# Optimization experiments

Measured on AMD Instinct MI355X. Metric: run time of the kernel, lower is better.

Reference implementation:

```python
import jax, jax.numpy as jnp
import numpy as np

PAD_TOKEN = -2.0
EPS = 1e-6
NEG_INF = -1.0e9


def _layer_norm(x, gamma, beta):
    mu = jnp.mean(x, axis=-1, keepdims=True)
    var = jnp.mean(jnp.square(x - mu), axis=-1, keepdims=True)
    return (x - mu) * jax.lax.rsqrt(var + EPS) * gamma + beta


def setup_inputs() -> dict:
    key = jax.random.key(0)
    ks = jax.random.split(key, 10)
    B, N, M, D, H, E, O = 128, 32, 384, 256, 8, 32, 256
    S = N + M
    x_pmhc = jax.random.normal(ks[0], (B, S, D), jnp.float32)
    # masks hold raw token values; PAD_TOKEN marks padding positions
    p_len = jax.random.randint(ks[1], (B,), 8, N + 1)
    m_len = jax.random.randint(ks[2], (B,), M // 2, M + 1)
    p_mask = jnp.where(jnp.arange(N)[None, :] < p_len[:, None], 1.0, PAD_TOKEN).astype(jnp.float32)
    m_mask = jnp.where(jnp.arange(M)[None, :] < m_len[:, None], 1.0, PAD_TOKEN).astype(jnp.float32)
    # learned params (keras random_normal init stddev=0.05; random_uniform in [-0.05, 0.05])
    q_proj = 0.05 * jax.random.normal(ks[3], (H, D, E), jnp.float32)
    k_proj = 0.05 * jax.random.normal(ks[4], (H, D, E), jnp.float32)
    v_proj = 0.05 * jax.random.normal(ks[5], (H, D, E), jnp.float32)
    g_proj = jax.random.uniform(ks[6], (H, D, E), jnp.float32, -0.05, 0.05)
    out_w = 0.05 * jax.random.normal(ks[7], (H * E, O), jnp.float32)
    out_b = jnp.zeros((O,), jnp.float32)
    ln1_g = jnp.ones((D,), jnp.float32)
    ln1_b = jnp.zeros((D,), jnp.float32)
    ln2_g = jnp.ones((O,), jnp.float32)
    ln2_b = jnp.zeros((O,), jnp.float32)
    return dict(x_pmhc=x_pmhc, p_mask=p_mask, m_mask=m_mask,
                q_proj=q_proj, k_proj=k_proj, v_proj=v_proj, g_proj=g_proj,
                out_w=out_w, out_b=out_b,
                ln1_g=ln1_g, ln1_b=ln1_b, ln2_g=ln2_g, ln2_b=ln2_b)


def _mask_2d(p, m):
    # p: [B,N] in {0,1}, m: [B,M] in {0,1}
    B, N = p.shape
    M = m.shape[1]
    cross_pm = p[:, :, None] * m[:, None, :]          # [B,N,M]
    cross_mp = m[:, :, None] * p[:, None, :]          # [B,M,N]
    top = jnp.concatenate([jnp.zeros((B, N, N), p.dtype), cross_pm], axis=2)
    bot = jnp.concatenate([cross_mp, jnp.zeros((B, M, M), p.dtype)], axis=2)
    return jnp.concatenate([top, bot], axis=1)        # [B,S,S]


def reference(x_pmhc, p_mask, m_mask, q_proj, k_proj, v_proj, g_proj,
              out_w, out_b, ln1_g, ln1_b, ln2_g, ln2_b):
    H, _, E = q_proj.shape
    B, S, _ = x_pmhc.shape
    scale = 1.0 / jnp.sqrt(jnp.asarray(E, jnp.float32))
    x = _layer_norm(x_pmhc, ln1_g, ln1_b)
    p = jnp.where(p_mask == PAD_TOKEN, 0.0, 1.0)
    m = jnp.where(m_mask == PAD_TOKEN, 0.0, 1.0)
    q = jnp.einsum('bxd,hde->bhxe', x, q_proj)
    k = jnp.einsum('bxd,hde->bhxe', x, k_proj)
    v = jnp.einsum('bxd,hde->bhxe', x, v_proj)
    g = jnp.einsum('bxd,hde->bhxe', x, g_proj)
    att = jnp.einsum('bhxe,bhye->bhxy', q, k) * scale          # [B,H,S,S]
    mask2d = _mask_2d(p, m)                                     # [B,S,S]
    att = jax.nn.softmax(att + ((1.0 - mask2d) * NEG_INF)[:, None], axis=-1)
    att = att * mask2d[:, None]
    out = jnp.einsum('bhxy,bhye->bhxe', att, v)
    out = out * jax.nn.sigmoid(g)
    out = out.transpose(0, 2, 1, 3).reshape(B, S, H * E)
    out = out @ out_w + out_b
    return _layer_norm(out, ln2_g, ln2_b)
```

## Files before the change

### kernel.cpp

```cpp
#include <hip/hip_runtime.h>

typedef unsigned short u16;
typedef __bf16 bf16x8 __attribute__((ext_vector_type(8)));
typedef float f32x4 __attribute__((ext_vector_type(4)));

#define B_    128
#define S_    416
#define NPEP  32
#define MMHC  384
#define D_    256
#define H_    8
#define E_    32
#define O_    256
#define BS_   (B_ * S_)

#define PAD_TOK (-2.0f)
#define SCALE_E 0.17677669529663687f

typedef const __attribute__((address_space(1))) void cg_void;
typedef __attribute__((address_space(3))) void lds_void;

__device__ __forceinline__ float bf2f(u16 u) {
  union { unsigned int i; float f; } x; x.i = ((unsigned int)u) << 16; return x.f;
}
__device__ __forceinline__ u16 f2bf(float f) {
  union { float f; unsigned int i; } x; x.f = f;
  unsigned int i = x.i;
  return (u16)((i + 0x7FFFu + ((i >> 16) & 1u)) >> 16);
}
__device__ __forceinline__ unsigned pk2bf(float lo, float hi) {
  return (unsigned)f2bf(lo) | ((unsigned)f2bf(hi) << 16);
}

__global__ __launch_bounds__(256)
void prep(const float* __restrict__ q, const float* __restrict__ k,
          const float* __restrict__ v, const float* __restrict__ g,
          const float* __restrict__ ow, u16* __restrict__ WT, u16* __restrict__ WoT,
          const float* __restrict__ x, u16* __restrict__ xln,
          const float* __restrict__ gam, const float* __restrict__ bet) {
  const int bx = blockIdx.x, t = threadIdx.x;
  if (bx < 1024) {
    const int col = bx;
    const int p = col >> 8, h = (col >> 5) & 7, e = col & 31;
    const float* src = (p == 0) ? q : (p == 1) ? k : (p == 2) ? v : g;
    WT[col * 256 + t] = f2bf(src[(h * 256 + t) * 32 + e]);
    return;
  }
  if (bx < 1280) {
    const int n = bx - 1024;
    WoT[n * 256 + t] = f2bf(ow[t * 256 + n]);
    return;
  }
  const int w = t >> 6, lane = t & 63;
  const size_t row = (size_t)(bx - 1280) * 4 + w;
  const float4 u = *((const float4*)x + row * 64 + lane);
  const float x0 = u.x, x1 = u.y, x2 = u.z, x3 = u.w;
  float sum = (x0 + x1) + (x2 + x3);
  float ss  = (x0 * x0 + x1 * x1) + (x2 * x2 + x3 * x3);
  #pragma unroll
  for (int off = 32; off; off >>= 1) {
    sum += __shfl_xor(sum, off);
    ss  += __shfl_xor(ss, off);
  }
  const float mean = sum * 0.00390625f;
  float var = ss * 0.00390625f - mean * mean;
  var = fmaxf(var, 0.0f);
  const float rs = rsqrtf(var + 1e-6f);
  const float4 g4 = *((const float4*)gam + lane);
  const float4 b4 = *((const float4*)bet + lane);
  ushort4 r;
  r.x = f2bf((x0 - mean) * rs * g4.x + b4.x);
  r.y = f2bf((x1 - mean) * rs * g4.y + b4.y);
  r.z = f2bf((x2 - mean) * rs * g4.z + b4.z);
  r.w = f2bf((x3 - mean) * rs * g4.w + b4.w);
  *((ushort4*)xln + row * 64 + lane) = r;
}

__global__ __launch_bounds__(256, 2)
void gemm_qkvg(const u16* __restrict__ A, const u16* __restrict__ BT,
               u16* __restrict__ Qh, u16* __restrict__ Kh,
               u16* __restrict__ Vh, u16* __restrict__ Gh) {
  __shared__ __attribute__((aligned(16))) u16 As[2][128 * 64];
  __shared__ __attribute__((aligned(16))) u16 Bs[2][128 * 64];
  const int L = blockIdx.x;
  const int m0 = ((L & 7) + 8 * (L >> 6)) * 128;
  const int n0 = ((L >> 3) & 7) * 128;
  const int tid = threadIdx.x;
  const int lane = tid & 63;
  const int w = tid >> 6;
  const int wr = (w >> 1) * 64;
  const int wc = (w & 1) * 64;
  const int mi = lane & 15;
  const int quad = lane >> 4;
  const int rseg = lane >> 3;
  const int gcol = (lane & 7) ^ rseg;

#define STAGE_G1(buf, kc)                                                      \
  {                                                                            \
    _Pragma("unroll")                                                          \
    for (int j = 0; j < 4; ++j) {                                              \
      const int seg = w * 4 + j;                                               \
      const int r = seg * 8 + rseg;                                            \
      const u16* ga = &A[(size_t)(m0 + r) * 256 + (kc) + gcol * 8];            \
      __builtin_amdgcn_global_load_lds((cg_void*)ga,                           \
          (lds_void*)&As[buf][seg * 512], 16, 0, 0);                           \
      const u16* gb = &BT[(size_t)(n0 + r) * 256 + (kc) + gcol * 8];           \
      __builtin_amdgcn_global_load_lds((cg_void*)gb,                           \
          (lds_void*)&Bs[buf][seg * 512], 16, 0, 0);                           \
    }                                                                          \
  }

  f32x4 acc[4][4] = {};
  STAGE_G1(0, 0);
  __syncthreads();
  #pragma unroll
  for (int kt8 = 0; kt8 < 4; ++kt8) {
    const int cur = kt8 & 1;
    if (kt8 < 3) STAGE_G1(cur ^ 1, (kt8 + 1) * 64);
    #pragma unroll
    for (int kt = 0; kt < 2; ++kt) {
      bf16x8 a[4], bb[4];
      #pragma unroll
      for (int i = 0; i < 4; ++i) {
        const int m = wr + i * 16 + mi;
        const int pg = (kt * 4 + quad) ^ (mi & 7);
        a[i] = *(const bf16x8*)&As[cur][m * 64 + pg * 8];
      }
      #pragma unroll
      for (int i = 0; i < 4; ++i) {
        const int n = wc + i * 16 + mi;
        const int pg = (kt * 4 + quad) ^ (mi & 7);
        bb[i] = *(const bf16x8*)&Bs[cur][n * 64 + pg * 8];
      }
      #pragma unroll
      for (int i = 0; i < 4; ++i)
        #pragma unroll
        for (int jn = 0; jn < 4; ++jn)
          acc[i][jn] = __builtin_amdgcn_mfma_f32_16x16x32_bf16(a[i], bb[jn], acc[i][jn], 0, 0, 0);
    }
    if (kt8 < 3) __syncthreads();
  }
#undef STAGE_G1
  u16* dstj[4];
  #pragma unroll
  for (int jn = 0; jn < 4; ++jn) {
    const int colb = n0 + wc + jn * 16;
    const int p = colb >> 8;
    const int h = (colb >> 5) & 7;
    const int e = (colb & 16) + mi;
    u16* bp = (p == 0) ? Qh : (p == 1) ? Kh : (p == 2) ? Vh : Gh;
    dstj[jn] = bp + (size_t)h * BS_ * 32 + e;
  }
  #pragma unroll
  for (int i = 0; i < 4; ++i) {
    const int row = m0 + wr + i * 16 + quad * 4;
    #pragma unroll
    for (int r = 0; r < 4; ++r) {
      #pragma unroll
      for (int jn = 0; jn < 4; ++jn)
        dstj[jn][(size_t)(row + r) * 32] = f2bf(acc[i][jn][r]);
    }
  }
}

__global__ __launch_bounds__(256, 4)
void att_fused(const u16* __restrict__ Qh, const u16* __restrict__ Kh,
               const u16* __restrict__ Vh, const u16* __restrict__ Gh,
               const float* __restrict__ p_mask, const float* __restrict__ m_mask,
               u16* __restrict__ atto) {
  __shared__ __attribute__((aligned(16))) u16 VT[32][392];
  __shared__ __attribute__((aligned(16))) u16 VpT[32][40];
  __shared__ __attribute__((aligned(16))) float pf[32];
  __shared__ __attribute__((aligned(16))) float mfl[384];
  const int bh = blockIdx.x;
  const int b = bh >> 3, h = bh & 7;
  const int t = threadIdx.x;
  const int lane = t & 63, w = t >> 6;
  const int mi = lane & 15, quad = lane >> 4;
  const size_t hb = (size_t)h * BS_ + (size_t)b * S_;

  if (t < 32) pf[t] = (p_mask[b * NPEP + t] == PAD_TOK) ? 0.0f : 1.0f;
  mfl[t] = (m_mask[b * MMHC + t] == PAD_TOK) ? 0.0f : 1.0f;
  if (t < 128) mfl[256 + t] = (m_mask[b * MMHC + 256 + t] == PAD_TOK) ? 0.0f : 1.0f;
  {
    const int y = t >> 3, e0 = (t & 7) * 4;
    const ushort4 u = *(const ushort4*)&Vh[(hb + y) * 32 + e0];
    VpT[e0 + 0][y] = u.x; VpT[e0 + 1][y] = u.y;
    VpT[e0 + 2][y] = u.z; VpT[e0 + 3][y] = u.w;
  }
  #pragma unroll
  for (int i = 0; i < 12; ++i) {
    const int idx = i * 256 + t;
    const int y = idx >> 3, e0 = (idx & 7) * 4;
    const ushort4 u = *(const ushort4*)&Vh[(hb + 32 + y) * 32 + e0];
    VT[e0 + 0][y] = u.x; VT[e0 + 1][y] = u.y;
    VT[e0 + 2][y] = u.z; VT[e0 + 3][y] = u.w;
  }
  __syncthreads();

  const f32x4 fz = {0.0f, 0.0f, 0.0f, 0.0f};
  const int idxA = ((quad & 1) * 2) * 16 + mi;
  const int idxB = idxA + 16;
  const bool hi = quad >= 2;
  union U8 { unsigned u[4]; bf16x8 v; };

  if (w < 2) {
    const bf16x8 aq = *(const bf16x8*)&Qh[(hb + w * 16 + mi) * 32 + quad * 8];
    float lsum = 0.0f;
    f32x4 o0 = fz, o1 = fz;
    #pragma unroll
    for (int ks = 0; ks < 12; ++ks) {
      unsigned pA0, pA1, pB0, pB1;
      {
        const int kt = 2 * ks;
        const bf16x8 bk = *(const bf16x8*)&Kh[(hb + 32 + kt * 16 + mi) * 32 + quad * 8];
        const f32x4 s = __builtin_amdgcn_mfma_f32_16x16x32_bf16(bk, aq, fz, 0, 0, 0);
        const float4 m4 = *(const float4*)&mfl[kt * 16 + quad * 4];
        const float e0 = m4.x * __expf(s[0] * SCALE_E);
        const float e1 = m4.y * __expf(s[1] * SCALE_E);
        const float e2 = m4.z * __expf(s[2] * SCALE_E);
        const float e3 = m4.w * __expf(s[3] * SCALE_E);
        lsum += (e0 + e1) + (e2 + e3);
        pA0 = pk2bf(e0, e1); pA1 = pk2bf(e2, e3);
      }
      {
        const int kt = 2 * ks + 1;
        const bf16x8 bk = *(const bf16x8*)&Kh[(hb + 32 + kt * 16 + mi) * 32 + quad * 8];
        const f32x4 s = __builtin_amdgcn_mfma_f32_16x16x32_bf16(bk, aq, fz, 0, 0, 0);
        const float4 m4 = *(const float4*)&mfl[kt * 16 + quad * 4];
        const float e0 = m4.x * __expf(s[0] * SCALE_E);
        const float e1 = m4.y * __expf(s[1] * SCALE_E);
        const float e2 = m4.z * __expf(s[2] * SCALE_E);
        const float e3 = m4.w * __expf(s[3] * SCALE_E);
        lsum += (e0 + e1) + (e2 + e3);
        pB0 = pk2bf(e0, e1); pB1 = pk2bf(e2, e3);
      }
      const unsigned a00 = __shfl(pA0, idxA), a01 = __shfl(pA1, idxA);
      const unsigned b00 = __shfl(pB0, idxA), b01 = __shfl(pB1, idxA);
      const unsigned a10 = __shfl(pA0, idxB), a11 = __shfl(pA1, idxB);
      const unsigned b10 = __shfl(pB0, idxB), b11 = __shfl(pB1, idxB);
      U8 pf_;
      pf_.u[0] = hi ? b00 : a00;
      pf_.u[1] = hi ? b01 : a01;
      pf_.u[2] = hi ? b10 : a10;
      pf_.u[3] = hi ? b11 : a11;
      const bf16x8 v0 = *(const bf16x8*)&VT[mi][ks * 32 + quad * 8];
      const bf16x8 v1 = *(const bf16x8*)&VT[16 + mi][ks * 32 + quad * 8];
      o0 = __builtin_amdgcn_mfma_f32_16x16x32_bf16(v0, pf_.v, o0, 0, 0, 0);
      o1 = __builtin_amdgcn_mfma_f32_16x16x32_bf16(v1, pf_.v, o1, 0, 0, 0);
    }
    lsum += __shfl_xor(lsum, 16);
    lsum += __shfl_xor(lsum, 32);
    const int prow = w * 16 + mi;
    const float sc = (1.0f / lsum) * pf[prow];
    const ushort4 g0 = *(const ushort4*)&Gh[(hb + prow) * 32 + quad * 4];
    const ushort4 g1 = *(const ushort4*)&Gh[(hb + prow) * 32 + 16 + quad * 4];
    ushort4 r0, r1;
    r0.x = f2bf(o0[0] * sc / (1.0f + __expf(-bf2f(g0.x))));
    r0.y = f2bf(o0[1] * sc / (1.0f + __expf(-bf2f(g0.y))));
    r0.z = f2bf(o0[2] * sc / (1.0f + __expf(-bf2f(g0.z))));
    r0.w = f2bf(o0[3] * sc / (1.0f + __expf(-bf2f(g0.w))));
    r1.x = f2bf(o1[0] * sc / (1.0f + __expf(-bf2f(g1.x))));
    r1.y = f2bf(o1[1] * sc / (1.0f + __expf(-bf2f(g1.y))));
    r1.z = f2bf(o1[2] * sc / (1.0f + __expf(-bf2f(g1.z))));
    r1.w = f2bf(o1[3] * sc / (1.0f + __expf(-bf2f(g1.w))));
    *(ushort4*)&atto[(hb + prow) * 32 + quad * 4] = r0;
    *(ushort4*)&atto[(hb + prow) * 32 + 16 + quad * 4] = r1;
  } else {
    const int wid = w - 2;
    const bf16x8 bk0 = *(const bf16x8*)&Kh[(hb + mi) * 32 + quad * 8];
    const bf16x8 bk1 = *(const bf16x8*)&Kh[(hb + 16 + mi) * 32 + quad * 8];
    const bf16x8 bv0 = *(const bf16x8*)&VpT[mi][quad * 8];
    const bf16x8 bv1 = *(const bf16x8*)&VpT[16 + mi][quad * 8];
    const float4 pfa = *(const float4*)&pf[quad * 4];
    const float4 pfb = *(const float4*)&pf[16 + quad * 4];
    for (int i = 0; i < 12; ++i) {
      const int rloc = (i * 2 + wid) * 16;
      const size_t grow = hb + 32 + rloc + mi;
      const bf16x8 aq = *(const bf16x8*)&Qh[grow * 32 + quad * 8];
      const f32x4 s0 = __builtin_amdgcn_mfma_f32_16x16x32_bf16(bk0, aq, fz, 0, 0, 0);
      const f32x4 s1 = __builtin_amdgcn_mfma_f32_16x16x32_bf16(bk1, aq, fz, 0, 0, 0);
      const float e00 = pfa.x * __expf(s0[0] * SCALE_E);
      const float e01 = pfa.y * __expf(s0[1] * SCALE_E);
      const float e02 = pfa.z * __expf(s0[2] * SCALE_E);
      const float e03 = pfa.w * __expf(s0[3] * SCALE_E);
      const float e10 = pfb.x * __expf(s1[0] * SCALE_E);
      const float e11 = pfb.y * __expf(s1[1] * SCALE_E);
      const float e12 = pfb.z * __expf(s1[2] * SCALE_E);
      const float e13 = pfb.w * __expf(s1[3] * SCALE_E);
      float lsum = ((e00 + e01) + (e02 + e03)) + ((e10 + e11) + (e12 + e13));
      lsum += __shfl_xor(lsum, 16);
      lsum += __shfl_xor(lsum, 32);
      const unsigned pA0 = pk2bf(e00, e01), pA1 = pk2bf(e02, e03);
      const unsigned pB0 = pk2bf(e10, e11), pB1 = pk2bf(e12, e13);
      const unsigned a00 = __shfl(pA0, idxA), a01 = __shfl(pA1, idxA);
      const unsigned b00 = __shfl(pB0, idxA), b01 = __shfl(pB1, idxA);
      const unsigned a10 = __shfl(pA0, idxB), a11 = __shfl(pA1, idxB);
      const unsigned b10 = __shfl(pB0, idxB), b11 = __shfl(pB1, idxB);
      U8 pf_;
      pf_.u[0] = hi ? b00 : a00;
      pf_.u[1] = hi ? b01 : a01;
      pf_.u[2] = hi ? b10 : a10;
      pf_.u[3] = hi ? b11 : a11;
      const f32x4 o0 = __builtin_amdgcn_mfma_f32_16x16x32_bf16(bv0, pf_.v, fz, 0, 0, 0);
      const f32x4 o1 = __builtin_amdgcn_mfma_f32_16x16x32_bf16(bv1, pf_.v, fz, 0, 0, 0);
      const float sc = (1.0f / lsum) * mfl[rloc + mi];
      const ushort4 g0 = *(const ushort4*)&Gh[grow * 32 + quad * 4];
      const ushort4 g1 = *(const ushort4*)&Gh[grow * 32 + 16 + quad * 4];
      ushort4 r0, r1;
      r0.x = f2bf(o0[0] * sc / (1.0f + __expf(-bf2f(g0.x))));
      r0.y = f2bf(o0[1] * sc / (1.0f + __expf(-bf2f(g0.y))));
      r0.z = f2bf(o0[2] * sc / (1.0f + __expf(-bf2f(g0.z))));
      r0.w = f2bf(o0[3] * sc / (1.0f + __expf(-bf2f(g0.w))));
      r1.x = f2bf(o1[0] * sc / (1.0f + __expf(-bf2f(g1.x))));
      r1.y = f2bf(o1[1] * sc / (1.0f + __expf(-bf2f(g1.y))));
      r1.z = f2bf(o1[2] * sc / (1.0f + __expf(-bf2f(g1.z))));
      r1.w = f2bf(o1[3] * sc / (1.0f + __expf(-bf2f(g1.w))));
      *(ushort4*)&atto[grow * 32 + quad * 4] = r0;
      *(ushort4*)&atto[grow * 32 + 16 + quad * 4] = r1;
    }
  }
}

__global__ __launch_bounds__(512, 2)
void gemm2_ln(const u16* __restrict__ A, const u16* __restrict__ BT,
              float* __restrict__ out, const float* __restrict__ bias,
              const float* __restrict__ gam, const float* __restrict__ bet) {
  __shared__ __attribute__((aligned(16))) u16 As[128 * 64];
  __shared__ __attribute__((aligned(16))) u16 Bs[256 * 64];
  __shared__ float rsum[128][4];
  __shared__ float rssq[128][4];
  __shared__ float mean_s[128], rstd_s[128];
  const int m0 = blockIdx.x * 128;
  const int tid = threadIdx.x;
  const int lane = tid & 63;
  const int w = tid >> 6;
  const int wr = (w >> 2) * 64;
  const int wc = (w & 3) * 64;
  const int mi = lane & 15;
  const int quad = lane >> 4;
  const int rseg = lane >> 3;
  const int gcol = (lane & 7) ^ rseg;
  f32x4 acc[4][4] = {};
  for (int kc = 0; kc < 256; kc += 64) {
    __syncthreads();
    #pragma unroll
    for (int j = 0; j < 2; ++j) {
      const int seg = w * 2 + j;
      const int r = seg * 8 + rseg;
      const int c = kc + gcol * 8;
      const u16* ga = &A[((size_t)(c >> 5) * BS_ + (m0 + r)) * 32 + (c & 31)];
      __builtin_amdgcn_global_load_lds((cg_void*)ga, (lds_void*)&As[seg * 512], 16, 0, 0);
    }
    #pragma unroll
    for (int j = 0; j < 4; ++j) {
      const int seg = w * 4 + j;
      const int r = seg * 8 + rseg;
      const u16* gb = &BT[(size_t)r * 256 + kc + gcol * 8];
      __builtin_amdgcn_global_load_lds((cg_void*)gb, (lds_void*)&Bs[seg * 512], 16, 0, 0);
    }
    __syncthreads();
    #pragma unroll
    for (int kt = 0; kt < 2; ++kt) {
      bf16x8 a[4], bb[4];
      #pragma unroll
      for (int i = 0; i < 4; ++i) {
        const int m = wr + i * 16 + mi;
        const int pg = (kt * 4 + quad) ^ (mi & 7);
        a[i] = *(const bf16x8*)&As[m * 64 + pg * 8];
      }
      #pragma unroll
      for (int i = 0; i < 4; ++i) {
        const int n = wc + i * 16 + mi;
        const int pg = (kt * 4 + quad) ^ (mi & 7);
        bb[i] = *(const bf16x8*)&Bs[n * 64 + pg * 8];
      }
      #pragma unroll
      for (int i = 0; i < 4; ++i)
        #pragma unroll
        for (int jn = 0; jn < 4; ++jn)
          acc[i][jn] = __builtin_amdgcn_mfma_f32_16x16x32_bf16(a[i], bb[jn], acc[i][jn], 0, 0, 0);
    }
  }
  float bia[4];
  #pragma unroll
  for (int jn = 0; jn < 4; ++jn) bia[jn] = bias[wc + jn * 16 + mi];
  #pragma unroll
  for (int i = 0; i < 4; ++i) {
    #pragma unroll
    for (int r = 0; r < 4; ++r) {
      float s = 0.0f, qq = 0.0f;
      #pragma unroll
      for (int jn = 0; jn < 4; ++jn) {
        const float v = acc[i][jn][r] + bia[jn];
        s += v; qq += v * v;
      }
      #pragma unroll
      for (int off = 1; off < 16; off <<= 1) {
        s  += __shfl_xor(s, off);
        qq += __shfl_xor(qq, off);
      }
      if (mi == 0) {
        const int rl = wr + i * 16 + quad * 4 + r;
        rsum[rl][w & 3] = s;
        rssq[rl][w & 3] = qq;
      }
    }
  }
  __syncthreads();
  if (tid < 128) {
    const float s = rsum[tid][0] + rsum[tid][1] + rsum[tid][2] + rsum[tid][3];
    const float qq = rssq[tid][0] + rssq[tid][1] + rssq[tid][2] + rssq[tid][3];
    const float mean = s * 0.00390625f;
    float var = qq * 0.00390625f - mean * mean;
    var = fmaxf(var, 0.0f);
    mean_s[tid] = mean;
    rstd_s[tid] = rsqrtf(var + 1e-6f);
  }
  __syncthreads();
  #pragma unroll
  for (int jn = 0; jn < 4; ++jn) {
    const int col = wc + jn * 16 + mi;
    const float gv = gam[col], bv = bet[col];
    #pragma unroll
    for (int i = 0; i < 4; ++i) {
      #pragma unroll
      for (int r = 0; r < 4; ++r) {
        const int rl = wr + i * 16 + quad * 4 + r;
        const float v = acc[i][jn][r] + bia[jn];
        out[(size_t)(m0 + rl) * 256 + col] = (v - mean_s[rl]) * rstd_s[rl] * gv + bv;
      }
    }
  }
}

extern "C" void kernel_launch(void* const* d_in, const int* in_sizes, int n_in,
                              void* d_out, int out_size, void* d_ws, size_t ws_size,
                              hipStream_t stream) {
  const float* x      = (const float*)d_in[0];
  const float* p_mask = (const float*)d_in[1];
  const float* m_mask = (const float*)d_in[2];
  const float* q_proj = (const float*)d_in[3];
  const float* k_proj = (const float*)d_in[4];
  const float* v_proj = (const float*)d_in[5];
  const float* g_proj = (const float*)d_in[6];
  const float* out_w  = (const float*)d_in[7];
  const float* out_b  = (const float*)d_in[8];
  const float* ln1_g  = (const float*)d_in[9];
  const float* ln1_b  = (const float*)d_in[10];
  const float* ln2_g  = (const float*)d_in[11];
  const float* ln2_b  = (const float*)d_in[12];

  char* ws = (char*)d_ws;
  u16* WT   = (u16*)(ws);
  u16* WoT  = (u16*)(ws + 524288);
  u16* attx = (u16*)(ws + 655360);
  u16* Qh   = (u16*)(ws + 27918336);
  u16* Kh   = (u16*)(ws + 55181312);
  u16* Vh   = (u16*)(ws + 82444288);
  u16* Gh   = (u16*)(ws + 109707264);
  float* outp = (float*)d_out;

  hipLaunchKernelGGL(prep, dim3(1280 + BS_ / 4), dim3(256), 0, stream,
                     q_proj, k_proj, v_proj, g_proj, out_w, WT, WoT,
                     x, attx, ln1_g, ln1_b);
  hipLaunchKernelGGL(gemm_qkvg, dim3(8 * (BS_ / 128)), dim3(256), 0, stream,
                     attx, WT, Qh, Kh, Vh, Gh);
  hipLaunchKernelGGL(att_fused, dim3(B_ * H_), dim3(256), 0, stream,
                     Qh, Kh, Vh, Gh, p_mask, m_mask, attx);
  hipLaunchKernelGGL(gemm2_ln, dim3(BS_ / 128), dim3(512), 0, stream,
                     attx, WoT, outp, out_b, ln2_g, ln2_b);
}
```

Baseline: 228.4 us.

## Load GEMM operands directly from global into registers, dropping LDS staging

Both the QKVG projection GEMM and the output GEMM+LayerNorm kernel stop staging A/B tiles through LDS with global_load_lds and barriers. Each wave now loads its MFMA fragments straight from global memory into registers, and the launch-bounds occupancy hint is raised from 2 to 4 blocks. The aim is to remove LDS traffic and barrier stalls and to raise occupancy so more waves hide latency. The cost is that operand data shared between waves is fetched repeatedly from global/L2, and the 16-byte per-lane fragment loads may coalesce poorly.

```diff
diff --git a/kernel.cpp b/kernel.cpp
--- a/kernel.cpp
+++ b/kernel.cpp
@@ -76,12 +76,10 @@
   *((ushort4*)xln + row * 64 + lane) = r;
 }
 
-__global__ __launch_bounds__(256, 2)
+__global__ __launch_bounds__(256, 4)
 void gemm_qkvg(const u16* __restrict__ A, const u16* __restrict__ BT,
                u16* __restrict__ Qh, u16* __restrict__ Kh,
                u16* __restrict__ Vh, u16* __restrict__ Gh) {
-  __shared__ __attribute__((aligned(16))) u16 As[2][128 * 64];
-  __shared__ __attribute__((aligned(16))) u16 Bs[2][128 * 64];
   const int L = blockIdx.x;
   const int m0 = ((L & 7) + 8 * (L >> 6)) * 128;
   const int n0 = ((L >> 3) & 7) * 128;
@@ -92,55 +90,24 @@
   const int wc = (w & 1) * 64;
   const int mi = lane & 15;
   const int quad = lane >> 4;
-  const int rseg = lane >> 3;
-  const int gcol = (lane & 7) ^ rseg;
-
-#define STAGE_G1(buf, kc)                                                      \
-  {                                                                            \
-    _Pragma("unroll")                                                          \
-    for (int j = 0; j < 4; ++j) {                                              \
-      const int seg = w * 4 + j;                                               \
-      const int r = seg * 8 + rseg;                                            \
-      const u16* ga = &A[(size_t)(m0 + r) * 256 + (kc) + gcol * 8];            \
-      __builtin_amdgcn_global_load_lds((cg_void*)ga,                           \
-          (lds_void*)&As[buf][seg * 512], 16, 0, 0);                           \
-      const u16* gb = &BT[(size_t)(n0 + r) * 256 + (kc) + gcol * 8];           \
-      __builtin_amdgcn_global_load_lds((cg_void*)gb,                           \
-          (lds_void*)&Bs[buf][seg * 512], 16, 0, 0);                           \
-    }                                                                          \
-  }
-
   f32x4 acc[4][4] = {};
-  STAGE_G1(0, 0);
-  __syncthreads();
-  #pragma unroll
-  for (int kt8 = 0; kt8 < 4; ++kt8) {
-    const int cur = kt8 & 1;
-    if (kt8 < 3) STAGE_G1(cur ^ 1, (kt8 + 1) * 64);
-    #pragma unroll
-    for (int kt = 0; kt < 2; ++kt) {
-      bf16x8 a[4], bb[4];
-      #pragma unroll
-      for (int i = 0; i < 4; ++i) {
-        const int m = wr + i * 16 + mi;
-        const int pg = (kt * 4 + quad) ^ (mi & 7);
-        a[i] = *(const bf16x8*)&As[cur][m * 64 + pg * 8];
-      }
-      #pragma unroll
-      for (int i = 0; i < 4; ++i) {
-        const int n = wc + i * 16 + mi;
-        const int pg = (kt * 4 + quad) ^ (mi & 7);
-        bb[i] = *(const bf16x8*)&Bs[cur][n * 64 + pg * 8];
-      }
-      #pragma unroll
-      for (int i = 0; i < 4; ++i)
-        #pragma unroll
-        for (int jn = 0; jn < 4; ++jn)
-          acc[i][jn] = __builtin_amdgcn_mfma_f32_16x16x32_bf16(a[i], bb[jn], acc[i][jn], 0, 0, 0);
-    }
-    if (kt8 < 3) __syncthreads();
-  }
-#undef STAGE_G1
+  const u16* Ab = A  + (size_t)(m0 + wr + mi) * 256 + quad * 8;
+  const u16* Bb = BT + (size_t)(n0 + wc + mi) * 256 + quad * 8;
+  #pragma unroll
+  for (int kk = 0; kk < 8; ++kk) {
+    bf16x8 a[4], bb[4];
+    #pragma unroll
+    for (int i = 0; i < 4; ++i)
+      a[i] = *(const bf16x8*)&Ab[i * 16 * 256 + kk * 32];
+    #pragma unroll
+    for (int i = 0; i < 4; ++i)
+      bb[i] = *(const bf16x8*)&Bb[i * 16 * 256 + kk * 32];
+    #pragma unroll
+    for (int i = 0; i < 4; ++i)
+      #pragma unroll
+      for (int jn = 0; jn < 4; ++jn)
+        acc[i][jn] = __builtin_amdgcn_mfma_f32_16x16x32_bf16(a[i], bb[jn], acc[i][jn], 0, 0, 0);
+  }
   u16* dstj[4];
   #pragma unroll
   for (int jn = 0; jn < 4; ++jn) {
@@ -322,12 +289,10 @@
   }
 }
 
-__global__ __launch_bounds__(512, 2)
+__global__ __launch_bounds__(512, 4)
 void gemm2_ln(const u16* __restrict__ A, const u16* __restrict__ BT,
               float* __restrict__ out, const float* __restrict__ bias,
               const float* __restrict__ gam, const float* __restrict__ bet) {
-  __shared__ __attribute__((aligned(16))) u16 As[128 * 64];
-  __shared__ __attribute__((aligned(16))) u16 Bs[256 * 64];
   __shared__ float rsum[128][4];
   __shared__ float rssq[128][4];
   __shared__ float mean_s[128], rstd_s[128];
@@ -339,48 +304,21 @@
   const int wc = (w & 3) * 64;
   const int mi = lane & 15;
   const int quad = lane >> 4;
-  const int rseg = lane >> 3;
-  const int gcol = (lane & 7) ^ rseg;
   f32x4 acc[4][4] = {};
-  for (int kc = 0; kc < 256; kc += 64) {
-    __syncthreads();
-    #pragma unroll
-    for (int j = 0; j < 2; ++j) {
-      const int seg = w * 2 + j;
-      const int r = seg * 8 + rseg;
-      const int c = kc + gcol * 8;
-      const u16* ga = &A[((size_t)(c >> 5) * BS_ + (m0 + r)) * 32 + (c & 31)];
-      __builtin_amdgcn_global_load_lds((cg_void*)ga, (lds_void*)&As[seg * 512], 16, 0, 0);
-    }
-    #pragma unroll
-    for (int j = 0; j < 4; ++j) {
-      const int seg = w * 4 + j;
-      const int r = seg * 8 + rseg;
-      const u16* gb = &BT[(size_t)r * 256 + kc + gcol * 8];
-      __builtin_amdgcn_global_load_lds((cg_void*)gb, (lds_void*)&Bs[seg * 512], 16, 0, 0);
-    }
-    __syncthreads();
-    #pragma unroll
-    for (int kt = 0; kt < 2; ++kt) {
-      bf16x8 a[4], bb[4];
-      #pragma unroll
-      for (int i = 0; i < 4; ++i) {
-        const int m = wr + i * 16 + mi;
-        const int pg = (kt * 4 + quad) ^ (mi & 7);
-        a[i] = *(const bf16x8*)&As[m * 64 + pg * 8];
-      }
-      #pragma unroll
-      for (int i = 0; i < 4; ++i) {
-        const int n = wc + i * 16 + mi;
-        const int pg = (kt * 4 + quad) ^ (mi & 7);
-        bb[i] = *(const bf16x8*)&Bs[n * 64 + pg * 8];
-      }
-      #pragma unroll
-      for (int i = 0; i < 4; ++i)
-        #pragma unroll
-        for (int jn = 0; jn < 4; ++jn)
-          acc[i][jn] = __builtin_amdgcn_mfma_f32_16x16x32_bf16(a[i], bb[jn], acc[i][jn], 0, 0, 0);
-    }
+  #pragma unroll
+  for (int kk = 0; kk < 8; ++kk) {
+    bf16x8 a[4], bb[4];
+    #pragma unroll
+    for (int i = 0; i < 4; ++i)
+      a[i] = *(const bf16x8*)&A[((size_t)kk * BS_ + (m0 + wr + i * 16 + mi)) * 32 + quad * 8];
+    #pragma unroll
+    for (int i = 0; i < 4; ++i)
+      bb[i] = *(const bf16x8*)&BT[(size_t)(wc + i * 16 + mi) * 256 + kk * 32 + quad * 8];
+    #pragma unroll
+    for (int i = 0; i < 4; ++i)
+      #pragma unroll
+      for (int jn = 0; jn < 4; ++jn)
+        acc[i][jn] = __builtin_amdgcn_mfma_f32_16x16x32_bf16(a[i], bb[jn], acc[i][jn], 0, 0, 0);
   }
   float bia[4];
   #pragma unroll
```

After: 322.6 us. 41.2% more time.
